# Performance work log

Measured on AMD Instinct MI355X. Metric: run time of the kernel, lower is better.

Reference implementation:

```python
import jax, jax.numpy as jnp
import numpy as np


def _rho(x):
    # sqrt(relu(x)) - sqrt(relu(-x)) == sign(x) * sqrt(|x|) (signed sqrt)
    return jnp.sign(x) * jnp.sqrt(jnp.abs(x))


def _forward(node, edge, embedding, Wq_w, Wq_b, Wk_w, Wk_b, Wew, Web, Wa,
             nt_w, nt_b, et_w, et_b, h1_w, h1_b, h2_w, h2_b):
    B, N, C = node.shape
    ED = edge.shape[-1]          # original edge_dim
    ED2 = 2 * ED                 # self.edge_dim
    ATT = Wq_w.shape[0] // ED2   # att_dim
    # single-query attention: Q from node 0 only
    q = (node[:, 0:1] @ Wq_w.T + Wq_b).reshape(B, 1, ATT, ED2)   # [B,1,A,ED2]
    k = (node @ Wk_w.T + Wk_b).reshape(B, N, ATT, ED2)           # [B,N,A,ED2]
    qk = jnp.einsum('bqae,bnae->bqne', q, k)                     # [B,1,N,ED2]
    e0 = edge[:, 0:1]                                            # [B,1,N,ED]
    h = jax.nn.gelu(
        _rho(qk[..., :ED] * (e0 @ Wew.T)) + e0 @ Web.T + qk[..., ED:]
        + embedding[:, 0:1],
        approximate=False)                                       # [B,1,N,ED]
    e = h[:, 0, 1:, :]                                           # [B,N-1,ED]
    # softmax over the node axis (permute->softmax(-1)->permute == axis=1)
    alphas = jax.nn.softmax(e @ Wa.T, axis=1)                    # [B,N-1,IN]
    et = (e @ et_w.T + et_b) * alphas                            # [B,N-1,IN]
    nt = (node[:, 1:] @ nt_w.T + nt_b) * alphas                  # [B,N-1,IN]
    # head FFN: Linear(2*IN->IN) -> GELU -> Linear(IN->IN)
    tmp = jax.nn.gelu(jnp.concatenate([et, nt], axis=-1) @ h1_w.T + h1_b,
                      approximate=False) @ h2_w.T + h2_b          # [B,N-1,IN]
    scaler = float(2.0 / np.sqrt(C))
    node_out = tmp.sum(axis=-2) * scaler                         # [B,IN]
    tmp_p = jnp.transpose(tmp, (0, 2, 1))[:, :, None, :]          # [B,IN,1,N-1]
    et_p = jnp.transpose(et, (0, 2, 1))[:, :, None, :]            # [B,IN,1,N-1]
    return (node_out, tmp_p, et_p)


def setup_inputs() -> dict:
    key = jax.random.key(0)
    ks = jax.random.split(key, 20)
    B, N, C = 4, 512, 128
    ED, IN, ATT = 64, 128, 8
    ED2 = 2 * ED
    r = lambda k, shp: jax.random.normal(k, shp, jnp.float32)
    w = lambda k, shp: r(k, shp) * float(1.0 / np.sqrt(shp[-1]))
    return dict(
        node=r(ks[0], (B, N, C)),
        edge=r(ks[1], (B, N, N, ED)),
        embedding=r(ks[2], (B, N, N, ED)),
        Wq_w=w(ks[3], (ED2 * ATT, C)), Wq_b=0.01 * r(ks[4], (ED2 * ATT,)),
        Wk_w=w(ks[5], (ED2 * ATT, C)), Wk_b=0.01 * r(ks[6], (ED2 * ATT,)),
        Wew=w(ks[7], (ED, ED)), Web=w(ks[8], (ED, ED)),
        Wa=w(ks[9], (IN, ED)),
        nt_w=w(ks[10], (IN, C)), nt_b=0.01 * r(ks[11], (IN,)),
        et_w=w(ks[12], (IN, ED)), et_b=0.01 * r(ks[13], (IN,)),
        h1_w=w(ks[14], (IN, 2 * IN)), h1_b=0.01 * r(ks[15], (IN,)),
        h2_w=w(ks[16], (IN, IN)), h2_b=0.01 * r(ks[17], (IN,)),
    )


def reference(node, edge, embedding, Wq_w, Wq_b, Wk_w, Wk_b, Wew, Web, Wa,
              nt_w, nt_b, et_w, et_b, h1_w, h1_b, h2_w, h2_b):
    return _forward(node, edge, embedding, Wq_w, Wq_b, Wk_w, Wk_b, Wew, Web,
                    Wa, nt_w, nt_b, et_w, et_b, h1_w, h1_b, h2_w, h2_b)
```

## Files before the change

### kernel.cpp

```cpp
#include <hip/hip_runtime.h>
#include <hip/hip_bf16.h>

static constexpr int Bc = 4, Nc = 512, Cc = 128, EDc = 64, ED2c = 128, ATTc = 8, INc = 128;
static constexpr int Mc = Nc - 1;

static constexpr int OFF_WCOMB = 0;
static constexpr int OFF_BCOMB = OFF_WCOMB + Bc*ED2c*Cc;
static constexpr int OFF_H     = OFF_BCOMB + Bc*ED2c;
static constexpr int OFF_MAX   = OFF_H + Bc*Nc*EDc;
static constexpr int OFF_DEN   = OFF_MAX + Bc*INc;
static constexpr int OFF_ACC   = OFF_DEN + Bc*INc;

static constexpr int OUT_TMP = Bc*INc;
static constexpr int OUT_ETP = OUT_TMP + Bc*INc*Mc;

__device__ __forceinline__ float gelu_f(float x){ return 0.5f*x*(1.0f + erff(x*0.70710678118654752f)); }
__device__ __forceinline__ float rho_f(float x){ return copysignf(sqrtf(fabsf(x)), x); }

__global__ void k1_qcomb(const float* __restrict__ node,
                         const float* __restrict__ Wq_w, const float* __restrict__ Wq_b,
                         const float* __restrict__ Wk_w, const float* __restrict__ Wk_b,
                         float* __restrict__ ws){
    int b = blockIdx.x;
    int t = threadIdx.x;
    __shared__ float node0[Cc];
    __shared__ float q[ATTc*ED2c];
    if (t < Cc) node0[t] = node[(b*Nc + 0)*Cc + t];
    __syncthreads();
    for (int row = t; row < ATTc*ED2c; row += 256){
        float acc = Wq_b[row];
        const float* wr = Wq_w + row*Cc;
        #pragma unroll 8
        for (int c = 0; c < Cc; ++c) acc += node0[c]*wr[c];
        q[row] = acc;
    }
    __syncthreads();
    float* Wcomb = ws + OFF_WCOMB + b*ED2c*Cc;
    for (int idx = t; idx < ED2c*Cc; idx += 256){
        int e = idx >> 7, c = idx & 127;
        float acc = 0.f;
        #pragma unroll
        for (int a = 0; a < ATTc; ++a)
            acc += q[a*ED2c + e] * Wk_w[(a*ED2c + e)*Cc + c];
        Wcomb[idx] = acc;
    }
    if (t < ED2c){
        float acc = 0.f;
        #pragma unroll
        for (int a = 0; a < ATTc; ++a) acc += q[a*ED2c + t]*Wk_b[a*ED2c + t];
        ws[OFF_BCOMB + b*ED2c + t] = acc;
    }
    if (t < INc) ws[OFF_ACC + b*INc + t] = 0.f;
}

__global__ void k2_h(const float* __restrict__ node,
                     const float* __restrict__ edge, const float* __restrict__ emb,
                     const float* __restrict__ Wew, const float* __restrict__ Web,
                     float* __restrict__ ws){
    int bn = blockIdx.x;
    int b = bn >> 9, n = bn & 511;
    int t = threadIdx.x;
    __shared__ float nrow[Cc], e0[EDc], em[EDc], qk[ED2c], ew[EDc], eb[EDc];
    nrow[t] = node[(b*Nc + n)*Cc + t];
    size_t eoff = ((size_t)b*Nc*Nc + n)*EDc;
    if (t < EDc) e0[t]     = edge[eoff + t];
    else         em[t-EDc] = emb[eoff + (t-EDc)];
    __syncthreads();
    {
        const float* Wc = ws + OFF_WCOMB + b*ED2c*Cc + t*Cc;
        float acc = ws[OFF_BCOMB + b*ED2c + t];
        #pragma unroll 8
        for (int c = 0; c < Cc; ++c) acc += nrow[c]*Wc[c];
        qk[t] = acc;
    }
    float dotv = 0.f;
    if (t < EDc){
        const float* w = Wew + t*EDc;
        #pragma unroll 8
        for (int c = 0; c < EDc; ++c) dotv += e0[c]*w[c];
        ew[t] = dotv;
    } else {
        int d = t - EDc;
        const float* w = Web + d*EDc;
        #pragma unroll 8
        for (int c = 0; c < EDc; ++c) dotv += e0[c]*w[c];
        eb[d] = dotv;
    }
    __syncthreads();
    if (t < EDc){
        float x = rho_f(qk[t]*ew[t]) + eb[t] + qk[EDc + t] + em[t];
        ws[OFF_H + (b*Nc + n)*EDc + t] = gelu_f(x);
    }
}

__global__ void k3_stats(const float* __restrict__ Wa, float* __restrict__ ws){
    int bj = blockIdx.x;
    int b = bj >> 7, j = bj & 127;
    int l = threadIdx.x;
    __shared__ float wa[EDc];
    if (l < EDc) wa[l] = Wa[j*EDc + l];
    __syncthreads();
    float sv[8];
    float mx = -1e30f;
    #pragma unroll
    for (int i = 0; i < 8; ++i){
        int m = l + i*64;
        float s = -1e30f;
        if (m < Mc){
            const float* hp = ws + OFF_H + (b*Nc + m + 1)*EDc;
            s = 0.f;
            #pragma unroll 8
            for (int d = 0; d < EDc; ++d) s += hp[d]*wa[d];
        }
        sv[i] = s;
        mx = fmaxf(mx, s);
    }
    #pragma unroll
    for (int off = 32; off > 0; off >>= 1) mx = fmaxf(mx, __shfl_xor(mx, off));
    float sum = 0.f;
    #pragma unroll
    for (int i = 0; i < 8; ++i) if (sv[i] > -1e29f) sum += expf(sv[i] - mx);
    #pragma unroll
    for (int off = 32; off > 0; off >>= 1) sum += __shfl_xor(sum, off);
    if (l == 0){ ws[OFF_MAX + bj] = mx; ws[OFF_DEN + bj] = 1.0f/sum; }
}

__global__ void __launch_bounds__(128) k4_mlp(const float* __restrict__ node,
                       const float* __restrict__ Wa,
                       const float* __restrict__ et_w, const float* __restrict__ et_b,
                       const float* __restrict__ nt_w, const float* __restrict__ nt_b,
                       const float* __restrict__ h1_w, const float* __restrict__ h1_b,
                       const float* __restrict__ h2_w, const float* __restrict__ h2_b,
                       float* __restrict__ ws, float* __restrict__ out){
    constexpr int TM = 8;
    int blk = blockIdx.x;
    int b = blk >> 6;
    int m0 = (blk & 63)*TM;
    int t = threadIdx.x;
    int nm = Mc - m0; if (nm > TM) nm = TM;
    __shared__ float esh[TM][EDc];
    __shared__ float nsh[TM][Cc];
    __shared__ float cat[TM][2*INc];
    __shared__ float gsh[TM][INc];
    for (int i = t; i < TM*EDc; i += 128){
        int mi = i >> 6, d = i & 63;
        int row = m0 + mi + 1; if (row > Nc-1) row = Nc-1;
        esh[mi][d] = ws[OFF_H + (b*Nc + row)*EDc + d];
    }
    for (int i = t; i < TM*Cc; i += 128){
        int mi = i >> 7, c = i & 127;
        int row = m0 + mi + 1; if (row > Nc-1) row = Nc-1;
        nsh[mi][c] = node[(b*Nc + row)*Cc + c];
    }
    __syncthreads();
    float mx  = ws[OFF_MAX + b*INc + t];
    float inv = ws[OFF_DEN + b*INc + t];
    float acc[TM];
    float alpha[TM];
    {
        #pragma unroll
        for (int mi = 0; mi < TM; ++mi) acc[mi] = 0.f;
        const float* w = Wa + t*EDc;
        for (int d = 0; d < EDc; ++d){
            float wv = w[d];
            #pragma unroll
            for (int mi = 0; mi < TM; ++mi) acc[mi] += esh[mi][d]*wv;
        }
        #pragma unroll
        for (int mi = 0; mi < TM; ++mi) alpha[mi] = expf(acc[mi] - mx)*inv;
    }
    {
        float bb = et_b[t];
        #pragma unroll
        for (int mi = 0; mi < TM; ++mi) acc[mi] = 0.f;
        const float* w = et_w + t*EDc;
        for (int c = 0; c < EDc; ++c){
            float wv = w[c];
            #pragma unroll
            for (int mi = 0; mi < TM; ++mi) acc[mi] += esh[mi][c]*wv;
        }
        #pragma unroll
        for (int mi = 0; mi < TM; ++mi){
            float v = (acc[mi] + bb)*alpha[mi];
            cat[mi][t] = v;
            if (mi < nm) out[OUT_ETP + (b*INc + t)*Mc + (m0 + mi)] = v;
        }
    }
    {
        float bb = nt_b[t];
        #pragma unroll
        for (int mi = 0; mi < TM; ++mi) acc[mi] = 0.f;
        const float* w = nt_w + t*Cc;
        for (int c = 0; c < Cc; ++c){
            float wv = w[c];
            #pragma unroll
            for (int mi = 0; mi < TM; ++mi) acc[mi] += nsh[mi][c]*wv;
        }
        #pragma unroll
        for (int mi = 0; mi < TM; ++mi) cat[mi][INc + t] = (acc[mi] + bb)*alpha[mi];
    }
    __syncthreads();
    {
        float bb = h1_b[t];
        #pragma unroll
        for (int mi = 0; mi < TM; ++mi) acc[mi] = 0.f;
        const float* w = h1_w + t*(2*INc);
        for (int c = 0; c < 2*INc; ++c){
            float wv = w[c];
            #pragma unroll
            for (int mi = 0; mi < TM; ++mi) acc[mi] += cat[mi][c]*wv;
        }
        #pragma unroll
        for (int mi = 0; mi < TM; ++mi) gsh[mi][t] = gelu_f(acc[mi] + bb);
    }
    __syncthreads();
    {
        float bb = h2_b[t];
        #pragma unroll
        for (int mi = 0; mi < TM; ++mi) acc[mi] = 0.f;
        const float* w = h2_w + t*INc;
        for (int c = 0; c < INc; ++c){
            float wv = w[c];
            #pragma unroll
            for (int mi = 0; mi < TM; ++mi) acc[mi] += gsh[mi][c]*wv;
        }
        float lsum = 0.f;
        #pragma unroll
        for (int mi = 0; mi < TM; ++mi){
            if (mi < nm){
                float v = acc[mi] + bb;
                out[OUT_TMP + (b*INc + t)*Mc + (m0 + mi)] = v;
                lsum += v;
            }
        }
        atomicAdd(&ws[OFF_ACC + b*INc + t], lsum);
    }
}

__global__ void k5_nodeout(const float* __restrict__ ws, float* __restrict__ out){
    int i = blockIdx.x*256 + threadIdx.x;
    if (i < Bc*INc) out[i] = ws[OFF_ACC + i]*0.17677669529663687f;
}

extern "C" void kernel_launch(void* const* d_in, const int* in_sizes, int n_in,
                              void* d_out, int out_size, void* d_ws, size_t ws_size,
                              hipStream_t stream){
    const float* node = (const float*)d_in[0];
    const float* edge = (const float*)d_in[1];
    const float* emb  = (const float*)d_in[2];
    const float* Wq_w = (const float*)d_in[3];
    const float* Wq_b = (const float*)d_in[4];
    const float* Wk_w = (const float*)d_in[5];
    const float* Wk_b = (const float*)d_in[6];
    const float* Wew  = (const float*)d_in[7];
    const float* Web  = (const float*)d_in[8];
    const float* Wa   = (const float*)d_in[9];
    const float* nt_w = (const float*)d_in[10];
    const float* nt_b = (const float*)d_in[11];
    const float* et_w = (const float*)d_in[12];
    const float* et_b = (const float*)d_in[13];
    const float* h1_w = (const float*)d_in[14];
    const float* h1_b = (const float*)d_in[15];
    const float* h2_w = (const float*)d_in[16];
    const float* h2_b = (const float*)d_in[17];
    float* ws = (float*)d_ws;
    float* out = (float*)d_out;

    k1_qcomb<<<Bc, 256, 0, stream>>>(node, Wq_w, Wq_b, Wk_w, Wk_b, ws);
    k2_h<<<Bc*Nc, 128, 0, stream>>>(node, edge, emb, Wew, Web, ws);
    k3_stats<<<Bc*INc, 64, 0, stream>>>(Wa, ws);
    k4_mlp<<<Bc*64, 128, 0, stream>>>(node, Wa, et_w, et_b, nt_w, nt_b,
                                      h1_w, h1_b, h2_w, h2_b, ws, out);
    k5_nodeout<<<2, 256, 0, stream>>>(ws, out);
}
```

Baseline: 542.7 us.

## Tile h computation over node rows, precompute attention logits, stage MLP weights in LDS

```diff
diff --git a/kernel.cpp b/kernel.cpp
--- a/kernel.cpp
+++ b/kernel.cpp
@@ -1,13 +1,13 @@
 #include <hip/hip_runtime.h>
-#include <hip/hip_bf16.h>
-
-static constexpr int Bc = 4, Nc = 512, Cc = 128, EDc = 64, ED2c = 128, ATTc = 8, INc = 128;
-static constexpr int Mc = Nc - 1;
+
+static constexpr int Bc=4, Nc=512, Cc=128, EDc=64, ED2c=128, ATTc=8, INc=128;
+static constexpr int Mc = Nc-1;
 
 static constexpr int OFF_WCOMB = 0;
 static constexpr int OFF_BCOMB = OFF_WCOMB + Bc*ED2c*Cc;
 static constexpr int OFF_H     = OFF_BCOMB + Bc*ED2c;
-static constexpr int OFF_MAX   = OFF_H + Bc*Nc*EDc;
+static constexpr int OFF_S     = OFF_H + Bc*Nc*EDc;
+static constexpr int OFF_MAX   = OFF_S + Bc*Mc*INc;
 static constexpr int OFF_DEN   = OFF_MAX + Bc*INc;
 static constexpr int OFF_ACC   = OFF_DEN + Bc*INc;
 
@@ -17,7 +17,7 @@
 __device__ __forceinline__ float gelu_f(float x){ return 0.5f*x*(1.0f + erff(x*0.70710678118654752f)); }
 __device__ __forceinline__ float rho_f(float x){ return copysignf(sqrtf(fabsf(x)), x); }
 
-__global__ void k1_qcomb(const float* __restrict__ node,
+__global__ void __launch_bounds__(256) k1_qcomb(const float* __restrict__ node,
                          const float* __restrict__ Wq_w, const float* __restrict__ Wq_b,
                          const float* __restrict__ Wk_w, const float* __restrict__ Wk_b,
                          float* __restrict__ ws){
@@ -25,14 +25,15 @@
     int t = threadIdx.x;
     __shared__ float node0[Cc];
     __shared__ float q[ATTc*ED2c];
-    if (t < Cc) node0[t] = node[(b*Nc + 0)*Cc + t];
-    __syncthreads();
-    for (int row = t; row < ATTc*ED2c; row += 256){
-        float acc = Wq_b[row];
-        const float* wr = Wq_w + row*Cc;
-        #pragma unroll 8
-        for (int c = 0; c < Cc; ++c) acc += node0[c]*wr[c];
-        q[row] = acc;
+    if (t < Cc) node0[t] = node[(size_t)(b*Nc)*Cc + t];
+    __syncthreads();
+    int w = t >> 6, l = t & 63;
+    for (int r = w*256; r < w*256 + 256; ++r){
+        const float2 wv = *reinterpret_cast<const float2*>(Wq_w + (size_t)r*Cc + 2*l);
+        float a = wv.x*node0[2*l] + wv.y*node0[2*l+1];
+        #pragma unroll
+        for (int off = 32; off; off >>= 1) a += __shfl_xor(a, off);
+        if (l == 0) q[r] = a + Wq_b[r];
     }
     __syncthreads();
     float* Wcomb = ws + OFF_WCOMB + b*ED2c*Cc;
@@ -41,7 +42,7 @@
         float acc = 0.f;
         #pragma unroll
         for (int a = 0; a < ATTc; ++a)
-            acc += q[a*ED2c + e] * Wk_w[(a*ED2c + e)*Cc + c];
+            acc += q[a*ED2c + e] * Wk_w[(size_t)(a*ED2c + e)*Cc + c];
         Wcomb[idx] = acc;
     }
     if (t < ED2c){
@@ -53,183 +54,288 @@
     if (t < INc) ws[OFF_ACC + b*INc + t] = 0.f;
 }
 
-__global__ void k2_h(const float* __restrict__ node,
-                     const float* __restrict__ edge, const float* __restrict__ emb,
-                     const float* __restrict__ Wew, const float* __restrict__ Web,
-                     float* __restrict__ ws){
-    int bn = blockIdx.x;
-    int b = bn >> 9, n = bn & 511;
+__device__ __forceinline__ void stage_rows(const float* __restrict__ src, int rs, int c0,
+                                           float (*W)[65], int rowbase, int nrows, int t){
+    int nf4 = nrows*16;
+    for (int f = t; f < nf4; f += 128){
+        int row = f >> 4, cp = (f & 15) << 2;
+        float4 v = *reinterpret_cast<const float4*>(src + (size_t)row*rs + c0 + cp);
+        float* d = &W[rowbase + row][cp];
+        d[0]=v.x; d[1]=v.y; d[2]=v.z; d[3]=v.w;
+    }
+}
+
+__global__ void __launch_bounds__(128) k2_h_s(const float* __restrict__ node,
+            const float* __restrict__ edge, const float* __restrict__ emb,
+            const float* __restrict__ Wew, const float* __restrict__ Web,
+            const float* __restrict__ Wa, float* __restrict__ ws){
+    __shared__ float Wsh[128][65];
+    __shared__ float nsh[8][128];
+    __shared__ float e0sh[8][64];
+    __shared__ float emsh[8][64];
+    __shared__ float qksh[8][128];
+    __shared__ float ewsh[8][64];
+    __shared__ float ebsh[8][64];
+    __shared__ float hsh[8][64];
+    int blk = blockIdx.x;
+    int b = blk >> 6, n0 = (blk & 63)*8;
     int t = threadIdx.x;
-    __shared__ float nrow[Cc], e0[EDc], em[EDc], qk[ED2c], ew[EDc], eb[EDc];
-    nrow[t] = node[(b*Nc + n)*Cc + t];
-    size_t eoff = ((size_t)b*Nc*Nc + n)*EDc;
-    if (t < EDc) e0[t]     = edge[eoff + t];
-    else         em[t-EDc] = emb[eoff + (t-EDc)];
-    __syncthreads();
-    {
-        const float* Wc = ws + OFF_WCOMB + b*ED2c*Cc + t*Cc;
-        float acc = ws[OFF_BCOMB + b*ED2c + t];
-        #pragma unroll 8
-        for (int c = 0; c < Cc; ++c) acc += nrow[c]*Wc[c];
-        qk[t] = acc;
-    }
-    float dotv = 0.f;
-    if (t < EDc){
-        const float* w = Wew + t*EDc;
-        #pragma unroll 8
-        for (int c = 0; c < EDc; ++c) dotv += e0[c]*w[c];
-        ew[t] = dotv;
-    } else {
-        int d = t - EDc;
-        const float* w = Web + d*EDc;
-        #pragma unroll 8
-        for (int c = 0; c < EDc; ++c) dotv += e0[c]*w[c];
-        eb[d] = dotv;
-    }
-    __syncthreads();
-    if (t < EDc){
-        float x = rho_f(qk[t]*ew[t]) + eb[t] + qk[EDc + t] + em[t];
-        ws[OFF_H + (b*Nc + n)*EDc + t] = gelu_f(x);
-    }
-}
-
-__global__ void k3_stats(const float* __restrict__ Wa, float* __restrict__ ws){
+    {
+        const float4* np = reinterpret_cast<const float4*>(node + (size_t)(b*Nc + n0)*Cc);
+        float4* ns = reinterpret_cast<float4*>(&nsh[0][0]);
+        ns[t] = np[t]; ns[t+128] = np[t+128];
+        const float4* ep = reinterpret_cast<const float4*>(edge + ((size_t)b*Nc*Nc + n0)*EDc);
+        reinterpret_cast<float4*>(&e0sh[0][0])[t] = ep[t];
+        const float4* mp = reinterpret_cast<const float4*>(emb + ((size_t)b*Nc*Nc + n0)*EDc);
+        reinterpret_cast<float4*>(&emsh[0][0])[t] = mp[t];
+    }
+    const float* WcombB = ws + OFF_WCOMB + b*ED2c*Cc;
+    stage_rows(WcombB, Cc, 0, Wsh, 0, 128, t);
+    __syncthreads();
+    float acc[8];
+    float bc = ws[OFF_BCOMB + b*ED2c + t];
+    #pragma unroll
+    for (int mi = 0; mi < 8; ++mi) acc[mi] = bc;
+    for (int c = 0; c < 64; c += 4){
+        float w0=Wsh[t][c], w1=Wsh[t][c+1], w2=Wsh[t][c+2], w3=Wsh[t][c+3];
+        #pragma unroll
+        for (int mi = 0; mi < 8; ++mi){
+            float4 nv = *reinterpret_cast<const float4*>(&nsh[mi][c]);
+            acc[mi] += nv.x*w0 + nv.y*w1 + nv.z*w2 + nv.w*w3;
+        }
+    }
+    __syncthreads();
+    stage_rows(WcombB, Cc, 64, Wsh, 0, 128, t);
+    __syncthreads();
+    for (int c = 0; c < 64; c += 4){
+        float w0=Wsh[t][c], w1=Wsh[t][c+1], w2=Wsh[t][c+2], w3=Wsh[t][c+3];
+        #pragma unroll
+        for (int mi = 0; mi < 8; ++mi){
+            float4 nv = *reinterpret_cast<const float4*>(&nsh[mi][64 + c]);
+            acc[mi] += nv.x*w0 + nv.y*w1 + nv.z*w2 + nv.w*w3;
+        }
+    }
+    #pragma unroll
+    for (int mi = 0; mi < 8; ++mi) qksh[mi][t] = acc[mi];
+    __syncthreads();
+    stage_rows(Wew, EDc, 0, Wsh, 0, 64, t);
+    stage_rows(Web, EDc, 0, Wsh, 64, 64, t);
+    __syncthreads();
+    {
+        float dv[8];
+        #pragma unroll
+        for (int mi = 0; mi < 8; ++mi) dv[mi] = 0.f;
+        for (int c = 0; c < 64; c += 4){
+            float w0=Wsh[t][c], w1=Wsh[t][c+1], w2=Wsh[t][c+2], w3=Wsh[t][c+3];
+            #pragma unroll
+            for (int mi = 0; mi < 8; ++mi){
+                float4 ev = *reinterpret_cast<const float4*>(&e0sh[mi][c]);
+                dv[mi] += ev.x*w0 + ev.y*w1 + ev.z*w2 + ev.w*w3;
+            }
+        }
+        int d = t & 63;
+        if (t < 64){
+            #pragma unroll
+            for (int mi = 0; mi < 8; ++mi) ewsh[mi][d] = dv[mi];
+        } else {
+            #pragma unroll
+            for (int mi = 0; mi < 8; ++mi) ebsh[mi][d] = dv[mi];
+        }
+    }
+    __syncthreads();
+    {
+        int d = t & 63, g = t >> 6;
+        #pragma unroll
+        for (int k = 0; k < 4; ++k){
+            int mi = g*4 + k;
+            float x = rho_f(qksh[mi][d]*ewsh[mi][d]) + ebsh[mi][d] + qksh[mi][64+d] + emsh[mi][d];
+            float h = gelu_f(x);
+            hsh[mi][d] = h;
+            ws[OFF_H + (size_t)(b*Nc + n0 + mi)*EDc + d] = h;
+        }
+    }
+    stage_rows(Wa, EDc, 0, Wsh, 0, 128, t);
+    __syncthreads();
+    #pragma unroll
+    for (int mi = 0; mi < 8; ++mi){
+        int m = n0 + mi - 1;
+        if (m < 0) continue;
+        float s = 0.f;
+        for (int c = 0; c < 64; c += 4){
+            float w0=Wsh[t][c], w1=Wsh[t][c+1], w2=Wsh[t][c+2], w3=Wsh[t][c+3];
+            float4 hv = *reinterpret_cast<const float4*>(&hsh[mi][c]);
+            s += hv.x*w0 + hv.y*w1 + hv.z*w2 + hv.w*w3;
+        }
+        ws[OFF_S + ((size_t)(b*Mc + m))*INc + t] = s;
+    }
+}
+
+__global__ void k3_stats(float* __restrict__ ws){
     int bj = blockIdx.x;
     int b = bj >> 7, j = bj & 127;
     int l = threadIdx.x;
-    __shared__ float wa[EDc];
-    if (l < EDc) wa[l] = Wa[j*EDc + l];
-    __syncthreads();
     float sv[8];
     float mx = -1e30f;
     #pragma unroll
     for (int i = 0; i < 8; ++i){
-        int m = l + i*64;
+        int m = i*64 + l;
         float s = -1e30f;
-        if (m < Mc){
-            const float* hp = ws + OFF_H + (b*Nc + m + 1)*EDc;
-            s = 0.f;
-            #pragma unroll 8
-            for (int d = 0; d < EDc; ++d) s += hp[d]*wa[d];
-        }
-        sv[i] = s;
-        mx = fmaxf(mx, s);
-    }
-    #pragma unroll
-    for (int off = 32; off > 0; off >>= 1) mx = fmaxf(mx, __shfl_xor(mx, off));
+        if (m < Mc) s = ws[OFF_S + ((size_t)(b*Mc + m))*INc + j];
+        sv[i] = s; mx = fmaxf(mx, s);
+    }
+    #pragma unroll
+    for (int off = 32; off; off >>= 1) mx = fmaxf(mx, __shfl_xor(mx, off));
     float sum = 0.f;
     #pragma unroll
     for (int i = 0; i < 8; ++i) if (sv[i] > -1e29f) sum += expf(sv[i] - mx);
     #pragma unroll
-    for (int off = 32; off > 0; off >>= 1) sum += __shfl_xor(sum, off);
+    for (int off = 32; off; off >>= 1) sum += __shfl_xor(sum, off);
     if (l == 0){ ws[OFF_MAX + bj] = mx; ws[OFF_DEN + bj] = 1.0f/sum; }
 }
 
+__device__ __forceinline__ void stage32(const float* __restrict__ src, int rs, int c0,
+                                        float (*W)[33], int t){
+    #pragma unroll
+    for (int rep = 0; rep < 8; ++rep){
+        int f = t + rep*128;
+        int row = f >> 3, cp = (f & 7) << 2;
+        float4 v = *reinterpret_cast<const float4*>(src + (size_t)row*rs + c0 + cp);
+        float* d = &W[row][cp];
+        d[0]=v.x; d[1]=v.y; d[2]=v.z; d[3]=v.w;
+    }
+}
+
 __global__ void __launch_bounds__(128) k4_mlp(const float* __restrict__ node,
-                       const float* __restrict__ Wa,
-                       const float* __restrict__ et_w, const float* __restrict__ et_b,
-                       const float* __restrict__ nt_w, const float* __restrict__ nt_b,
-                       const float* __restrict__ h1_w, const float* __restrict__ h1_b,
-                       const float* __restrict__ h2_w, const float* __restrict__ h2_b,
-                       float* __restrict__ ws, float* __restrict__ out){
-    constexpr int TM = 8;
+        const float* __restrict__ et_w, const float* __restrict__ et_b,
+        const float* __restrict__ nt_w, const float* __restrict__ nt_b,
+        const float* __restrict__ h1_w, const float* __restrict__ h1_b,
+        const float* __restrict__ h2_w, const float* __restrict__ h2_b,
+        float* __restrict__ ws, float* __restrict__ out){
+    constexpr int TM = 4;
+    __shared__ float Wsh[128][33];
+    __shared__ float esh[TM][64];
+    __shared__ float nsh[TM][128];
+    __shared__ float csh[TM][256];
+    __shared__ float gsh[TM][128];
     int blk = blockIdx.x;
-    int b = blk >> 6;
-    int m0 = (blk & 63)*TM;
+    int b = blk >> 7, m0 = (blk & 127)*TM;
     int t = threadIdx.x;
     int nm = Mc - m0; if (nm > TM) nm = TM;
-    __shared__ float esh[TM][EDc];
-    __shared__ float nsh[TM][Cc];
-    __shared__ float cat[TM][2*INc];
-    __shared__ float gsh[TM][INc];
-    for (int i = t; i < TM*EDc; i += 128){
-        int mi = i >> 6, d = i & 63;
-        int row = m0 + mi + 1; if (row > Nc-1) row = Nc-1;
-        esh[mi][d] = ws[OFF_H + (b*Nc + row)*EDc + d];
-    }
-    for (int i = t; i < TM*Cc; i += 128){
-        int mi = i >> 7, c = i & 127;
-        int row = m0 + mi + 1; if (row > Nc-1) row = Nc-1;
-        nsh[mi][c] = node[(b*Nc + row)*Cc + c];
-    }
-    __syncthreads();
+    if (m0 + TM <= Nc - 1){
+        const float4* hp = reinterpret_cast<const float4*>(ws + OFF_H + (size_t)(b*Nc + m0 + 1)*EDc);
+        if (t < 64) reinterpret_cast<float4*>(&esh[0][0])[t] = hp[t];
+        const float4* np = reinterpret_cast<const float4*>(node + (size_t)(b*Nc + m0 + 1)*Cc);
+        reinterpret_cast<float4*>(&nsh[0][0])[t] = np[t];
+    } else {
+        for (int i = t; i < TM*EDc; i += 128){
+            int mi = i >> 6, row = m0 + mi + 1; if (row > Nc-1) row = Nc-1;
+            esh[mi][i & 63] = ws[OFF_H + (size_t)(b*Nc + row)*EDc + (i & 63)];
+        }
+        for (int i = t; i < TM*Cc; i += 128){
+            int mi = i >> 7, row = m0 + mi + 1; if (row > Nc-1) row = Nc-1;
+            nsh[mi][i & 127] = node[(size_t)(b*Nc + row)*Cc + (i & 127)];
+        }
+    }
     float mx  = ws[OFF_MAX + b*INc + t];
     float inv = ws[OFF_DEN + b*INc + t];
+    float alpha[TM];
+    #pragma unroll
+    for (int mi = 0; mi < TM; ++mi){
+        float a = 0.f;
+        if (mi < nm){
+            float s = ws[OFF_S + ((size_t)(b*Mc + m0 + mi))*INc + t];
+            a = expf(s - mx)*inv;
+        }
+        alpha[mi] = a;
+    }
     float acc[TM];
-    float alpha[TM];
-    {
-        #pragma unroll
-        for (int mi = 0; mi < TM; ++mi) acc[mi] = 0.f;
-        const float* w = Wa + t*EDc;
-        for (int d = 0; d < EDc; ++d){
-            float wv = w[d];
-            #pragma unroll
-            for (int mi = 0; mi < TM; ++mi) acc[mi] += esh[mi][d]*wv;
-        }
-        #pragma unroll
-        for (int mi = 0; mi < TM; ++mi) alpha[mi] = expf(acc[mi] - mx)*inv;
+    #pragma unroll
+    for (int mi = 0; mi < TM; ++mi) acc[mi] = 0.f;
+    for (int cc = 0; cc < 64; cc += 32){
+        __syncthreads();
+        stage32(et_w, EDc, cc, Wsh, t);
+        __syncthreads();
+        for (int c = 0; c < 32; c += 4){
+            float w0=Wsh[t][c], w1=Wsh[t][c+1], w2=Wsh[t][c+2], w3=Wsh[t][c+3];
+            #pragma unroll
+            for (int mi = 0; mi < TM; ++mi){
+                float4 v = *reinterpret_cast<const float4*>(&esh[mi][cc + c]);
+                acc[mi] += v.x*w0 + v.y*w1 + v.z*w2 + v.w*w3;
+            }
+        }
     }
     {
         float bb = et_b[t];
-        #pragma unroll
-        for (int mi = 0; mi < TM; ++mi) acc[mi] = 0.f;
-        const float* w = et_w + t*EDc;
-        for (int c = 0; c < EDc; ++c){
-            float wv = w[c];
-            #pragma unroll
-            for (int mi = 0; mi < TM; ++mi) acc[mi] += esh[mi][c]*wv;
-        }
         #pragma unroll
         for (int mi = 0; mi < TM; ++mi){
             float v = (acc[mi] + bb)*alpha[mi];
-            cat[mi][t] = v;
-            if (mi < nm) out[OUT_ETP + (b*INc + t)*Mc + (m0 + mi)] = v;
+            csh[mi][t] = v;
+            if (mi < nm) out[OUT_ETP + (size_t)(b*INc + t)*Mc + (m0 + mi)] = v;
+        }
+    }
+    #pragma unroll
+    for (int mi = 0; mi < TM; ++mi) acc[mi] = 0.f;
+    for (int cc = 0; cc < 128; cc += 32){
+        __syncthreads();
+        stage32(nt_w, Cc, cc, Wsh, t);
+        __syncthreads();
+        for (int c = 0; c < 32; c += 4){
+            float w0=Wsh[t][c], w1=Wsh[t][c+1], w2=Wsh[t][c+2], w3=Wsh[t][c+3];
+            #pragma unroll
+            for (int mi = 0; mi < TM; ++mi){
+                float4 v = *reinterpret_cast<const float4*>(&nsh[mi][cc + c]);
+                acc[mi] += v.x*w0 + v.y*w1 + v.z*w2 + v.w*w3;
+            }
         }
     }
     {
         float bb = nt_b[t];
         #pragma unroll
-        for (int mi = 0; mi < TM; ++mi) acc[mi] = 0.f;
-        const float* w = nt_w + t*Cc;
-        for (int c = 0; c < Cc; ++c){
-            float wv = w[c];
-            #pragma unroll
-            for (int mi = 0; mi < TM; ++mi) acc[mi] += nsh[mi][c]*wv;
-        }
-        #pragma unroll
-        for (int mi = 0; mi < TM; ++mi) cat[mi][INc + t] = (acc[mi] + bb)*alpha[mi];
-    }
-    __syncthreads();
+        for (int mi = 0; mi < TM; ++mi) csh[mi][INc + t] = (acc[mi] + bb)*alpha[mi];
+    }
+    #pragma unroll
+    for (int mi = 0; mi < TM; ++mi) acc[mi] = 0.f;
+    for (int cc = 0; cc < 256; cc += 32){
+        __syncthreads();
+        stage32(h1_w, 2*INc, cc, Wsh, t);
+        __syncthreads();
+        for (int c = 0; c < 32; c += 4){
+            float w0=Wsh[t][c], w1=Wsh[t][c+1], w2=Wsh[t][c+2], w3=Wsh[t][c+3];
+            #pragma unroll
+            for (int mi = 0; mi < TM; ++mi){
+                float4 v = *reinterpret_cast<const float4*>(&csh[mi][cc + c]);
+                acc[mi] += v.x*w0 + v.y*w1 + v.z*w2 + v.w*w3;
+            }
+        }
+    }
     {
         float bb = h1_b[t];
         #pragma unroll
-        for (int mi = 0; mi < TM; ++mi) acc[mi] = 0.f;
-        const float* w = h1_w + t*(2*INc);
-        for (int c = 0; c < 2*INc; ++c){
-            float wv = w[c];
-            #pragma unroll
-            for (int mi = 0; mi < TM; ++mi) acc[mi] += cat[mi][c]*wv;
-        }
-        #pragma unroll
         for (int mi = 0; mi < TM; ++mi) gsh[mi][t] = gelu_f(acc[mi] + bb);
     }
-    __syncthreads();
+    #pragma unroll
+    for (int mi = 0; mi < TM; ++mi) acc[mi] = 0.f;
+    for (int cc = 0; cc < 128; cc += 32){
+        __syncthreads();
+        stage32(h2_w, INc, cc, Wsh, t);
+        __syncthreads();
+        for (int c = 0; c < 32; c += 4){
+            float w0=Wsh[t][c], w1=Wsh[t][c+1], w2=Wsh[t][c+2], w3=Wsh[t][c+3];
+            #pragma unroll
+            for (int mi = 0; mi < TM; ++mi){
+                float4 v = *reinterpret_cast<const float4*>(&gsh[mi][cc + c]);
+                acc[mi] += v.x*w0 + v.y*w1 + v.z*w2 + v.w*w3;
+            }
+        }
+    }
     {
         float bb = h2_b[t];
-        #pragma unroll
-        for (int mi = 0; mi < TM; ++mi) acc[mi] = 0.f;
-        const float* w = h2_w + t*INc;
-        for (int c = 0; c < INc; ++c){
-            float wv = w[c];
-            #pragma unroll
-            for (int mi = 0; mi < TM; ++mi) acc[mi] += gsh[mi][c]*wv;
-        }
         float lsum = 0.f;
         #pragma unroll
         for (int mi = 0; mi < TM; ++mi){
             if (mi < nm){
                 float v = acc[mi] + bb;
-                out[OUT_TMP + (b*INc + t)*Mc + (m0 + mi)] = v;
+                out[OUT_TMP + (size_t)(b*INc + t)*Mc + (m0 + mi)] = v;
                 lsum += v;
             }
         }
@@ -267,9 +373,9 @@
     float* out = (float*)d_out;
 
     k1_qcomb<<<Bc, 256, 0, stream>>>(node, Wq_w, Wq_b, Wk_w, Wk_b, ws);
-    k2_h<<<Bc*Nc, 128, 0, stream>>>(node, edge, emb, Wew, Web, ws);
-    k3_stats<<<Bc*INc, 64, 0, stream>>>(Wa, ws);
-    k4_mlp<<<Bc*64, 128, 0, stream>>>(node, Wa, et_w, et_b, nt_w, nt_b,
-                                      h1_w, h1_b, h2_w, h2_b, ws, out);
+    k2_h_s<<<Bc*64, 128, 0, stream>>>(node, edge, emb, Wew, Web, Wa, ws);
+    k3_stats<<<Bc*INc, 64, 0, stream>>>(ws);
+    k4_mlp<<<Bc*128, 128, 0, stream>>>(node, et_w, et_b, nt_w, nt_b,
+                                       h1_w, h1_b, h2_w, h2_b, ws, out);
     k5_nodeout<<<2, 256, 0, stream>>>(ws, out);
 }
```

After: 746.9 us. 37.6% more time.
